# Kernel optimization log

Hardware: AMD Instinct MI355X
Metric: run time of the kernel (lower is better)

Reference implementation:

```python
import jax, jax.numpy as jnp
import numpy as np

N_USERS = 100000
N_ITEMS = 50000
N_NODES = N_USERS + N_ITEMS
DIM = 64
N_EDGES = 1200000
BATCH = 4096


def _propagate(edge_index, emb):
    # row = source, col = destination (out[dst] += norm * emb[src])
    row, col = edge_index[0], edge_index[1]
    n = emb.shape[0]
    # degree counted over row occurrences only (faithful to `degree(row, ...)`)
    deg = jax.ops.segment_sum(jnp.ones_like(row, dtype=emb.dtype), row, num_segments=n)
    dinv = jnp.where(deg > 0, deg ** -0.5, 0.0).astype(emb.dtype)
    norm = dinv[row] * dinv[col]  # [E]
    msgs = norm[:, None] * emb[row]  # [E, D] gather + scale
    return jax.ops.segment_sum(msgs, col, num_segments=n)  # scatter-add into dst


def setup_inputs() -> dict:
    key = jax.random.key(0)
    ks = jax.random.split(key, 10)
    xavier = (6.0 / (N_USERS + DIM)) ** 0.5  # approximate xavier bounds per table
    user_emb = jax.random.uniform(ks[0], (N_USERS, DIM), jnp.float32, -xavier, xavier)
    xavier_i = (6.0 / (N_ITEMS + DIM)) ** 0.5
    item_emb = jax.random.uniform(ks[1], (N_ITEMS, DIM), jnp.float32, -xavier_i, xavier_i)
    lim = (1.0 / DIM) ** 0.5
    W1 = jax.random.uniform(ks[2], (DIM, DIM), jnp.float32, -lim, lim)
    b1 = jax.random.uniform(ks[3], (DIM,), jnp.float32, -lim, lim)
    W2 = jax.random.uniform(ks[4], (DIM, DIM), jnp.float32, -lim, lim)
    b2 = jax.random.uniform(ks[5], (DIM,), jnp.float32, -lim, lim)
    users = jax.random.randint(ks[6], (BATCH,), 0, N_USERS)
    items = jax.random.randint(ks[7], (BATCH,), 0, N_ITEMS)
    edge_index = jax.random.randint(ks[8], (2, N_EDGES), 0, N_NODES)
    return {"users": users, "items": items, "edge_index": edge_index,
            "user_emb": user_emb, "item_emb": item_emb,
            "W1": W1, "b1": b1, "W2": W2, "b2": b2}


def reference(users, items, edge_index, user_emb, item_emb, W1, b1, W2, b2):
    all_emb = jnp.concatenate([user_emb, item_emb], axis=0)  # [N, D]
    # layer 0: propagate -> linear -> relu
    all_emb = _propagate(edge_index, all_emb)
    all_emb = jax.nn.relu(all_emb @ W1.T + b1)
    # layer 1 (last): propagate -> linear (no relu)
    all_emb = _propagate(edge_index, all_emb)
    all_emb = all_emb @ W2.T + b2
    user_final = all_emb[:N_USERS]
    item_final = all_emb[N_USERS:]
    scores = jnp.sum(user_final[users] * item_final[items], axis=1)  # [B]
    return scores
```

## Files before the change

### kernel.cpp

```cpp
#include <hip/hip_runtime.h>
#include <math.h>

constexpr int NU = 100000;
constexpr int NI = 50000;
constexpr int NN = 150000;
constexpr int D  = 64;
constexpr int NE = 1200000;
constexpr int NE4 = NE / 4;
constexpr int B  = 4096;
constexpr int CAPB = 64;
constexpr int CAP2 = 40;

constexpr int NCHUNK = 3;
constexpr int CHUNK  = 65536;
constexpr int CWORDS = CHUNK / 4;
constexpr int WORDS  = 37504;
constexpr int RWORDS = 37500;
constexpr int NSLICE = 80;
constexpr int SLICE4 = NE4 / NSLICE;

constexpr int BMW = 4704;
constexpr int ZINTS = 167904;
constexpr int ZN4   = ZINTS / 4;


__global__ void k_zero(int4* __restrict__ p) {
    const int i = blockIdx.x * blockDim.x + threadIdx.x;
    if (i < ZN4) p[i] = make_int4(0, 0, 0, 0);
}

__global__ void k_flag(const int* __restrict__ users, const int* __restrict__ items,
                       unsigned int* __restrict__ bm0, int* __restrict__ bidx,
                       int* __restrict__ nb) {
    const int t = blockIdx.x * blockDim.x + threadIdx.x;
    if (t >= 2 * B) return;
    const int node = (t < B) ? users[t] : items[t - B] + NU;
    const unsigned int old = atomicOr(&bm0[node >> 5], 1u << (node & 31));
    if (!((old >> (node & 31)) & 1)) bidx[node] = atomicAdd(nb, 1);
}

__global__ void __launch_bounds__(256) k_hist(const int* __restrict__ row,
                                              unsigned int* __restrict__ hcopy) {
    __shared__ unsigned int lh[CWORDS];
    const int ci = blockIdx.x / NSLICE;
    const int si = blockIdx.x % NSLICE;
    const int lo = ci * CHUNK;
    const int cw = (ci == NCHUNK - 1) ? (WORDS - (NCHUNK - 1) * CWORDS) : CWORDS;
    for (int w = threadIdx.x; w < cw; w += 256) lh[w] = 0;
    __syncthreads();
    const int4* r4 = reinterpret_cast<const int4*>(row) + (size_t)si * SLICE4;
    const unsigned int span = (unsigned)(cw * 4);
    for (int t = threadIdx.x; t < SLICE4; t += 256) {
        const int4 r = r4[t];
        int v;
        v = r.x - lo; if ((unsigned)v < span) atomicAdd(&lh[v >> 2], 1u << (8 * (v & 3)));
        v = r.y - lo; if ((unsigned)v < span) atomicAdd(&lh[v >> 2], 1u << (8 * (v & 3)));
        v = r.z - lo; if ((unsigned)v < span) atomicAdd(&lh[v >> 2], 1u << (8 * (v & 3)));
        v = r.w - lo; if ((unsigned)v < span) atomicAdd(&lh[v >> 2], 1u << (8 * (v & 3)));
    }
    __syncthreads();
    unsigned int* dst = hcopy + (size_t)si * WORDS + ci * CWORDS;
    for (int w = threadIdx.x; w < cw; w += 256) dst[w] = lh[w];
}

__global__ void k_mark(const int* __restrict__ row, const int* __restrict__ col,
                       const unsigned int* __restrict__ bm0,
                       const int* __restrict__ bidx,
                       int* __restrict__ cntBd, int* __restrict__ csrBd,
                       unsigned int* __restrict__ bm1) {
    const int t = blockIdx.x * blockDim.x + threadIdx.x;
    if (t >= NE4) return;
    const int4 r = reinterpret_cast<const int4*>(row)[t];
    const int4 c = reinterpret_cast<const int4*>(col)[t];
    #define E1(rr, cc) if ((bm0[(cc) >> 5] >> ((cc) & 31)) & 1) { \
        const int bi = bidx[cc]; \
        const int s = atomicAdd(&cntBd[bi], 1); \
        csrBd[bi * CAPB + s] = rr; \
        atomicOr(&bm1[(rr) >> 5], 1u << ((rr) & 31)); }
    E1(r.x, c.x) E1(r.y, c.y) E1(r.z, c.z) E1(r.w, c.w)
    #undef E1
}

__global__ void k_dinvc(const unsigned int* __restrict__ hcopy,
                        float* __restrict__ dinv,
                        const unsigned int* __restrict__ bm1,
                        int* __restrict__ list, int* __restrict__ ncnt) {
    const int w = blockIdx.x * blockDim.x + threadIdx.x;
    if (w >= RWORDS) return;
    unsigned int s = 0;
    #pragma unroll 8
    for (int si = 0; si < NSLICE; ++si) s += hcopy[(size_t)si * WORDS + w];
    const int d0 = s & 255, d1 = (s >> 8) & 255, d2 = (s >> 16) & 255, d3 = (int)(s >> 24);
    float4 dv;
    dv.x = d0 > 0 ? 1.0f / sqrtf((float)d0) : 0.0f;
    dv.y = d1 > 0 ? 1.0f / sqrtf((float)d1) : 0.0f;
    dv.z = d2 > 0 ? 1.0f / sqrtf((float)d2) : 0.0f;
    dv.w = d3 > 0 ? 1.0f / sqrtf((float)d3) : 0.0f;
    reinterpret_cast<float4*>(dinv)[w] = dv;
    const unsigned int bits = (bm1[w >> 3] >> ((w & 7) * 4)) & 0xFu;
    const int n0 = w * 4;
    if (bits & 1u) list[atomicAdd(ncnt, 1)] = n0;
    if (bits & 2u) list[atomicAdd(ncnt, 1)] = n0 + 1;
    if (bits & 4u) list[atomicAdd(ncnt, 1)] = n0 + 2;
    if (bits & 8u) list[atomicAdd(ncnt, 1)] = n0 + 3;
}

__global__ void k_pass2(const int* __restrict__ row, const int* __restrict__ col,
                        const unsigned int* __restrict__ bm1,
                        int* __restrict__ cnt2d, int* __restrict__ csr2d) {
    const int t = blockIdx.x * blockDim.x + threadIdx.x;
    if (t >= NE4) return;
    const int4 r = reinterpret_cast<const int4*>(row)[t];
    const int4 c = reinterpret_cast<const int4*>(col)[t];
    #define E2(rr, cc) if ((bm1[(cc) >> 5] >> ((cc) & 31)) & 1) { \
        const int s = atomicAdd(&cnt2d[cc], 1); \
        csr2d[cc * CAP2 + s] = rr; }
    E2(r.x, c.x) E2(r.y, c.y) E2(r.z, c.z) E2(r.w, c.w)
    #undef E2
}

__global__ void k_gather1(const int* __restrict__ list, const int* __restrict__ ncnt,
                          const int* __restrict__ cnt2d, const int* __restrict__ csr2d,
                          const float* __restrict__ dinv,
                          const float* __restrict__ embU, const float* __restrict__ embI,
                          float* __restrict__ out) {
    const int lane = threadIdx.x & 63;
    const int idx = blockIdx.x * (blockDim.x >> 6) + (threadIdx.x >> 6);
    if (idx >= *ncnt) return;
    const int c = list[idx];
    const int ne = cnt2d[c];
    const int* es = csr2d + (size_t)c * CAP2;
    float a0 = 0.0f, a1 = 0.0f, a2 = 0.0f, a3 = 0.0f;
    int e = 0;
    for (; e + 3 < ne; e += 4) {
        const int4 r = *reinterpret_cast<const int4*>(es + e);
        const float d0 = dinv[r.x], d1 = dinv[r.y], d2 = dinv[r.z], d3 = dinv[r.w];
        const float* s0 = (r.x < NU) ? embU + (size_t)r.x * D : embI + (size_t)(r.x - NU) * D;
        const float* s1 = (r.y < NU) ? embU + (size_t)r.y * D : embI + (size_t)(r.y - NU) * D;
        const float* s2 = (r.z < NU) ? embU + (size_t)r.z * D : embI + (size_t)(r.z - NU) * D;
        const float* s3 = (r.w < NU) ? embU + (size_t)r.w * D : embI + (size_t)(r.w - NU) * D;
        a0 = fmaf(d0, s0[lane], a0);
        a1 = fmaf(d1, s1[lane], a1);
        a2 = fmaf(d2, s2[lane], a2);
        a3 = fmaf(d3, s3[lane], a3);
    }
    for (; e < ne; ++e) {
        const int r = es[e];
        const float* s = (r < NU) ? embU + (size_t)r * D : embI + (size_t)(r - NU) * D;
        a0 = fmaf(dinv[r], s[lane], a0);
    }
    out[(size_t)c * D + lane] = dinv[c] * ((a0 + a1) + (a2 + a3));
}

__global__ void __launch_bounds__(256) k_mlp_relu(const int* __restrict__ list,
                                                  const int* __restrict__ ncnt,
                                                  float* __restrict__ emb,
                                                  const float* __restrict__ W,
                                                  const float* __restrict__ b) {
    const int lane = threadIdx.x & 63;
    float w[D];
    #pragma unroll
    for (int k4 = 0; k4 < D / 4; ++k4) {
        const float4 v = *reinterpret_cast<const float4*>(W + (size_t)lane * D + k4 * 4);
        w[k4 * 4 + 0] = v.x; w[k4 * 4 + 1] = v.y;
        w[k4 * 4 + 2] = v.z; w[k4 * 4 + 3] = v.w;
    }
    const float bias = b[lane];

    const int n = *ncnt;
    const int wid = blockIdx.x * (blockDim.x >> 6) + (threadIdx.x >> 6);
    const int nw  = gridDim.x * (blockDim.x >> 6);
    for (int i4 = wid * 4; i4 < n; i4 += nw * 4) {
        const int r0 = list[i4];
        const int r1 = (i4 + 1 < n) ? list[i4 + 1] : r0;
        const int r2 = (i4 + 2 < n) ? list[i4 + 2] : r0;
        const int r3 = (i4 + 3 < n) ? list[i4 + 3] : r0;
        float* x0 = emb + (size_t)r0 * D;
        float* x1 = emb + (size_t)r1 * D;
        float* x2 = emb + (size_t)r2 * D;
        float* x3 = emb + (size_t)r3 * D;
        const float xv0 = x0[lane], xv1 = x1[lane], xv2 = x2[lane], xv3 = x3[lane];
        float a0 = bias, a1 = bias, a2 = bias, a3 = bias;
        #pragma unroll
        for (int k = 0; k < D; ++k) {
            const float wk = w[k];
            a0 = fmaf(__int_as_float(__builtin_amdgcn_readlane(__float_as_int(xv0), k)), wk, a0);
            a1 = fmaf(__int_as_float(__builtin_amdgcn_readlane(__float_as_int(xv1), k)), wk, a1);
            a2 = fmaf(__int_as_float(__builtin_amdgcn_readlane(__float_as_int(xv2), k)), wk, a2);
            a3 = fmaf(__int_as_float(__builtin_amdgcn_readlane(__float_as_int(xv3), k)), wk, a3);
        }
        x0[lane] = fmaxf(a0, 0.0f);
        x1[lane] = fmaxf(a1, 0.0f);
        x2[lane] = fmaxf(a2, 0.0f);
        x3[lane] = fmaxf(a3, 0.0f);
    }
}

__global__ void __launch_bounds__(256) k_score2(const int* __restrict__ users,
                                                const int* __restrict__ items,
                                                const int* __restrict__ bidx,
                                                const int* __restrict__ cntBd,
                                                const int* __restrict__ csrBd,
                                                const float* __restrict__ dinv,
                                                const float* __restrict__ embA,
                                                const float* __restrict__ W,
                                                const float* __restrict__ b,
                                                float* __restrict__ out) {
    __shared__ float sy[2][2][D];
    const int lane = threadIdx.x & 63;
    const int wid  = threadIdx.x >> 6;
    const int pp   = wid >> 1;
    const int t    = wid & 1;
    const int p    = blockIdx.x * 2 + pp;

    float w[D];
    #pragma unroll
    for (int k4 = 0; k4 < D / 4; ++k4) {
        const float4 v = *reinterpret_cast<const float4*>(W + (size_t)lane * D + k4 * 4);
        w[k4 * 4 + 0] = v.x; w[k4 * 4 + 1] = v.y;
        w[k4 * 4 + 2] = v.z; w[k4 * 4 + 3] = v.w;
    }

    const int c  = (t == 0) ? users[p] : items[p] + NU;
    const int bi = bidx[c];
    const int n  = cntBd[bi];
    const int* es = csrBd + (size_t)bi * CAPB;
    float a0 = 0.0f, a1 = 0.0f, a2 = 0.0f, a3 = 0.0f;
    int e = 0;
    for (; e + 3 < n; e += 4) {
        const int4 r = *reinterpret_cast<const int4*>(es + e);
        a0 = fmaf(dinv[r.x], embA[(size_t)r.x * D + lane], a0);
        a1 = fmaf(dinv[r.y], embA[(size_t)r.y * D + lane], a1);
        a2 = fmaf(dinv[r.z], embA[(size_t)r.z * D + lane], a2);
        a3 = fmaf(dinv[r.w], embA[(size_t)r.w * D + lane], a3);
    }
    for (; e < n; ++e) {
        const int r = es[e];
        a0 = fmaf(dinv[r], embA[(size_t)r * D + lane], a0);
    }
    const float x = dinv[c] * ((a0 + a1) + (a2 + a3));

    float y = b[lane];
    #pragma unroll
    for (int k = 0; k < D; ++k)
        y = fmaf(__int_as_float(__builtin_amdgcn_readlane(__float_as_int(x), k)),
                 w[k], y);
    sy[pp][t][lane] = y;
    __syncthreads();
    if (t == 0) {
        float prod = sy[pp][0][lane] * sy[pp][1][lane];
        #pragma unroll
        for (int off = 32; off >= 1; off >>= 1) prod += __shfl_down(prod, off, 64);
        if (lane == 0) out[p] = prod;
    }
}

extern "C" void kernel_launch(void* const* d_in, const int* in_sizes, int n_in,
                              void* d_out, int out_size, void* d_ws, size_t ws_size,
                              hipStream_t stream) {
    const int*   users    = (const int*)d_in[0];
    const int*   items    = (const int*)d_in[1];
    const int*   edge     = (const int*)d_in[2];
    const float* user_emb = (const float*)d_in[3];
    const float* item_emb = (const float*)d_in[4];
    const float* W1       = (const float*)d_in[5];
    const float* b1       = (const float*)d_in[6];
    const float* W2       = (const float*)d_in[7];
    const float* b2       = (const float*)d_in[8];
    float*       out      = (float*)d_out;

    const int* row  = edge;
    const int* colp = edge + NE;

    unsigned int* bm0   = (unsigned int*)d_ws;
    unsigned int* bm1   = (unsigned int*)d_ws + 4704;
    int*   cnt2d = (int*)d_ws + 9408;
    int*   cntBd = (int*)d_ws + 159424;
    int*   nb    = (int*)d_ws + 167872;
    int*   ncnt  = (int*)d_ws + 167888;
    float* dinv  = (float*)d_ws + 167904;
    int*   bidx  = (int*)d_ws + 317920;
    int*   list  = (int*)d_ws + 467936;
    int*   csrBd = (int*)d_ws + 617952;
    int*   csr2d = (int*)d_ws + 1158624;
    float* embA  = (float*)d_ws + 7159264;
    unsigned int* hcopy = (unsigned int*)csr2d;

    k_zero <<<(ZN4 + 255) / 256, 256, 0, stream>>>((int4*)d_ws);

    k_flag <<<(2 * B + 255) / 256, 256, 0, stream>>>(users, items, bm0, bidx, nb);
    k_hist <<<NCHUNK * NSLICE, 256, 0, stream>>>(row, hcopy);
    k_mark <<<(NE4 + 255) / 256, 256, 0, stream>>>(row, colp, bm0, bidx, cntBd, csrBd, bm1);
    k_dinvc<<<(RWORDS + 255) / 256, 256, 0, stream>>>(hcopy, dinv, bm1, list, ncnt);
    k_pass2<<<(NE4 + 255) / 256, 256, 0, stream>>>(row, colp, bm1, cnt2d, csr2d);

    k_gather1 <<<(NN + 3) / 4, 256, 0, stream>>>(list, ncnt, cnt2d, csr2d, dinv,
                                                 user_emb, item_emb, embA);
    k_mlp_relu<<<2048, 256, 0, stream>>>(list, ncnt, embA, W1, b1);
    k_score2<<<B / 2, 256, 0, stream>>>(users, items, bidx, cntBd, csrBd, dinv, embA,
                                        W2, b2, out);
}
```

Measured before the change: 172.1 us.

## Drop zero kernel, build batch bitmap in shared memory, grid-stride gather

Removes the standalone zeroing kernel. k_flag now builds the batch bitmap and unique counter in LDS with a single 1024-thread block and writes them out, so bm0 and nb no longer need pre-zeroing. The remaining zeroing of bm1, cnt2d, cntBd and ncnt is folded into k_hist, with the workspace layout reordered so those buffers are contiguous. k_gather1 switches from one wave per possible node (about 37.5k blocks) to a fixed 8192-block grid-stride loop over the active list. This saves a launch and many idle blocks, but the single-block flag kernel serializes that small step.

New measurement: 167.1 us. -2.9%, faster.

```diff
diff --git a/kernel.cpp b/kernel.cpp
--- a/kernel.cpp
+++ b/kernel.cpp
@@ -20,27 +20,35 @@
 constexpr int SLICE4 = NE4 / NSLICE;
 
 constexpr int BMW = 4704;
-constexpr int ZINTS = 167904;
-constexpr int ZN4   = ZINTS / 4;
-
-
-__global__ void k_zero(int4* __restrict__ p) {
-    const int i = blockIdx.x * blockDim.x + threadIdx.x;
-    if (i < ZN4) p[i] = make_int4(0, 0, 0, 0);
-}
-
-__global__ void k_flag(const int* __restrict__ users, const int* __restrict__ items,
-                       unsigned int* __restrict__ bm0, int* __restrict__ bidx,
-                       int* __restrict__ nb) {
-    const int t = blockIdx.x * blockDim.x + threadIdx.x;
-    if (t >= 2 * B) return;
-    const int node = (t < B) ? users[t] : items[t - B] + NU;
-    const unsigned int old = atomicOr(&bm0[node >> 5], 1u << (node & 31));
-    if (!((old >> (node & 31)) & 1)) bidx[node] = atomicAdd(nb, 1);
+constexpr int HZ4 = 163184 / 4;
+
+
+__global__ void __launch_bounds__(1024) k_flag(const int* __restrict__ users,
+                                               const int* __restrict__ items,
+                                               unsigned int* __restrict__ bm0,
+                                               int* __restrict__ bidx,
+                                               int* __restrict__ nb) {
+    __shared__ unsigned int sbm[BMW];
+    __shared__ int snb;
+    for (int i = threadIdx.x; i < BMW; i += 1024) sbm[i] = 0;
+    if (threadIdx.x == 0) snb = 0;
+    __syncthreads();
+    for (int t = threadIdx.x; t < 2 * B; t += 1024) {
+        const int node = (t < B) ? users[t] : items[t - B] + NU;
+        const unsigned int old = atomicOr(&sbm[node >> 5], 1u << (node & 31));
+        if (!((old >> (node & 31)) & 1)) bidx[node] = atomicAdd(&snb, 1);
+    }
+    __syncthreads();
+    for (int i = threadIdx.x; i < BMW; i += 1024) bm0[i] = sbm[i];
+    if (threadIdx.x == 0) *nb = snb;
 }
 
 __global__ void __launch_bounds__(256) k_hist(const int* __restrict__ row,
-                                              unsigned int* __restrict__ hcopy) {
+                                              unsigned int* __restrict__ hcopy,
+                                              int4* __restrict__ zbase) {
+    for (int i = blockIdx.x * 256 + threadIdx.x; i < HZ4; i += gridDim.x * 256)
+        zbase[i] = make_int4(0, 0, 0, 0);
+
     __shared__ unsigned int lh[CWORDS];
     const int ci = blockIdx.x / NSLICE;
     const int si = blockIdx.x % NSLICE;
@@ -125,31 +133,34 @@
                           const float* __restrict__ embU, const float* __restrict__ embI,
                           float* __restrict__ out) {
     const int lane = threadIdx.x & 63;
-    const int idx = blockIdx.x * (blockDim.x >> 6) + (threadIdx.x >> 6);
-    if (idx >= *ncnt) return;
-    const int c = list[idx];
-    const int ne = cnt2d[c];
-    const int* es = csr2d + (size_t)c * CAP2;
-    float a0 = 0.0f, a1 = 0.0f, a2 = 0.0f, a3 = 0.0f;
-    int e = 0;
-    for (; e + 3 < ne; e += 4) {
-        const int4 r = *reinterpret_cast<const int4*>(es + e);
-        const float d0 = dinv[r.x], d1 = dinv[r.y], d2 = dinv[r.z], d3 = dinv[r.w];
-        const float* s0 = (r.x < NU) ? embU + (size_t)r.x * D : embI + (size_t)(r.x - NU) * D;
-        const float* s1 = (r.y < NU) ? embU + (size_t)r.y * D : embI + (size_t)(r.y - NU) * D;
-        const float* s2 = (r.z < NU) ? embU + (size_t)r.z * D : embI + (size_t)(r.z - NU) * D;
-        const float* s3 = (r.w < NU) ? embU + (size_t)r.w * D : embI + (size_t)(r.w - NU) * D;
-        a0 = fmaf(d0, s0[lane], a0);
-        a1 = fmaf(d1, s1[lane], a1);
-        a2 = fmaf(d2, s2[lane], a2);
-        a3 = fmaf(d3, s3[lane], a3);
-    }
-    for (; e < ne; ++e) {
-        const int r = es[e];
-        const float* s = (r < NU) ? embU + (size_t)r * D : embI + (size_t)(r - NU) * D;
-        a0 = fmaf(dinv[r], s[lane], a0);
-    }
-    out[(size_t)c * D + lane] = dinv[c] * ((a0 + a1) + (a2 + a3));
+    const int n = *ncnt;
+    const int nwv = gridDim.x * (blockDim.x >> 6);
+    for (int idx = blockIdx.x * (blockDim.x >> 6) + (threadIdx.x >> 6);
+         idx < n; idx += nwv) {
+        const int c = list[idx];
+        const int ne = cnt2d[c];
+        const int* es = csr2d + (size_t)c * CAP2;
+        float a0 = 0.0f, a1 = 0.0f, a2 = 0.0f, a3 = 0.0f;
+        int e = 0;
+        for (; e + 3 < ne; e += 4) {
+            const int4 r = *reinterpret_cast<const int4*>(es + e);
+            const float d0 = dinv[r.x], d1 = dinv[r.y], d2 = dinv[r.z], d3 = dinv[r.w];
+            const float* s0 = (r.x < NU) ? embU + (size_t)r.x * D : embI + (size_t)(r.x - NU) * D;
+            const float* s1 = (r.y < NU) ? embU + (size_t)r.y * D : embI + (size_t)(r.y - NU) * D;
+            const float* s2 = (r.z < NU) ? embU + (size_t)r.z * D : embI + (size_t)(r.z - NU) * D;
+            const float* s3 = (r.w < NU) ? embU + (size_t)r.w * D : embI + (size_t)(r.w - NU) * D;
+            a0 = fmaf(d0, s0[lane], a0);
+            a1 = fmaf(d1, s1[lane], a1);
+            a2 = fmaf(d2, s2[lane], a2);
+            a3 = fmaf(d3, s3[lane], a3);
+        }
+        for (; e < ne; ++e) {
+            const int r = es[e];
+            const float* s = (r < NU) ? embU + (size_t)r * D : embI + (size_t)(r - NU) * D;
+            a0 = fmaf(dinv[r], s[lane], a0);
+        }
+        out[(size_t)c * D + lane] = dinv[c] * ((a0 + a1) + (a2 + a3));
+    }
 }
 
 __global__ void __launch_bounds__(256) k_mlp_relu(const int* __restrict__ list,
@@ -272,12 +283,12 @@
     const int* row  = edge;
     const int* colp = edge + NE;
 
-    unsigned int* bm0   = (unsigned int*)d_ws;
-    unsigned int* bm1   = (unsigned int*)d_ws + 4704;
-    int*   cnt2d = (int*)d_ws + 9408;
-    int*   cntBd = (int*)d_ws + 159424;
-    int*   nb    = (int*)d_ws + 167872;
-    int*   ncnt  = (int*)d_ws + 167888;
+    unsigned int* bm1   = (unsigned int*)d_ws;
+    int*   cnt2d = (int*)d_ws + 4704;
+    int*   cntBd = (int*)d_ws + 154720;
+    int*   ncnt  = (int*)d_ws + 163168;
+    unsigned int* bm0   = (unsigned int*)d_ws + 163184;
+    int*   nb    = (int*)d_ws + 167888;
     float* dinv  = (float*)d_ws + 167904;
     int*   bidx  = (int*)d_ws + 317920;
     int*   list  = (int*)d_ws + 467936;
@@ -286,16 +297,14 @@
     float* embA  = (float*)d_ws + 7159264;
     unsigned int* hcopy = (unsigned int*)csr2d;
 
-    k_zero <<<(ZN4 + 255) / 256, 256, 0, stream>>>((int4*)d_ws);
-
-    k_flag <<<(2 * B + 255) / 256, 256, 0, stream>>>(users, items, bm0, bidx, nb);
-    k_hist <<<NCHUNK * NSLICE, 256, 0, stream>>>(row, hcopy);
+    k_flag <<<1, 1024, 0, stream>>>(users, items, bm0, bidx, nb);
+    k_hist <<<NCHUNK * NSLICE, 256, 0, stream>>>(row, hcopy, (int4*)d_ws);
     k_mark <<<(NE4 + 255) / 256, 256, 0, stream>>>(row, colp, bm0, bidx, cntBd, csrBd, bm1);
     k_dinvc<<<(RWORDS + 255) / 256, 256, 0, stream>>>(hcopy, dinv, bm1, list, ncnt);
     k_pass2<<<(NE4 + 255) / 256, 256, 0, stream>>>(row, colp, bm1, cnt2d, csr2d);
 
-    k_gather1 <<<(NN + 3) / 4, 256, 0, stream>>>(list, ncnt, cnt2d, csr2d, dinv,
-                                                 user_emb, item_emb, embA);
+    k_gather1 <<<8192, 256, 0, stream>>>(list, ncnt, cnt2d, csr2d, dinv,
+                                         user_emb, item_emb, embA);
     k_mlp_relu<<<2048, 256, 0, stream>>>(list, ncnt, embA, W1, b1);
     k_score2<<<B / 2, 256, 0, stream>>>(users, items, bidx, cntBd, csrBd, dinv, embA,
                                         W2, b2, out);
```
